# Performance work log

Hardware: AMD Instinct MI355X
Metric: run time of the kernel (lower is better)

## Reference

```python
import jax, jax.numpy as jnp
import numpy as np

EMBED_DIM = 768
VOCAB = 4096
HID = 128
B, N = 8, 4096


def setup_inputs() -> dict:
    key = jax.random.key(0)
    ks = jax.random.split(key, 12)
    s = lambda k, sh, fan_in: jax.random.normal(k, sh, jnp.float32) * (1.0 / np.sqrt(fan_in))
    return {
        "coordinates": jax.random.normal(ks[0], (B, N, 2), jnp.float32),
        "features": jax.random.normal(ks[1], (B, N, 10), jnp.float32),
        # spatial encoder: Linear(2,128) -> ReLU -> Linear(128,768); weights stored [in,out]
        "Ws1": s(ks[2], (2, HID), 2), "bs1": jnp.zeros((HID,), jnp.float32),
        "Ws2": s(ks[3], (HID, EMBED_DIM), HID), "bs2": jnp.zeros((EMBED_DIM,), jnp.float32),
        # feature encoder: Linear(10,128) -> ReLU -> Linear(128,768)
        "Wf1": s(ks[4], (10, HID), 10), "bf1": jnp.zeros((HID,), jnp.float32),
        "Wf2": s(ks[5], (HID, EMBED_DIM), HID), "bf2": jnp.zeros((EMBED_DIM,), jnp.float32),
        # quantizer codebook (nn.Embedding weight)
        "codebook": jax.random.normal(ks[6], (VOCAB, EMBED_DIM), jnp.float32),
    }


def reference(coordinates, features, Ws1, bs1, Ws2, bs2, Wf1, bf1, Wf2, bf2, codebook):
    spatial_emb = jax.nn.relu(coordinates @ Ws1 + bs1) @ Ws2 + bs2   # [B,N,D]
    feature_emb = jax.nn.relu(features @ Wf1 + bf1) @ Wf2 + bf2     # [B,N,D]
    combined = spatial_emb + feature_emb                             # [B,N,D]
    # squared euclidean distances (argmin is invariant to sqrt / -||x||^2 term)
    x_sq = jnp.sum(combined * combined, axis=-1, keepdims=True)      # [B,N,1]
    c_sq = jnp.sum(codebook * codebook, axis=-1)                     # [V]
    dots = jnp.einsum('bnd,vd->bnv', combined, codebook)             # [B,N,V]
    dists = x_sq - 2.0 * dots + c_sq                                 # [B,N,V]
    tokens = jnp.argmin(dists, axis=-1)                              # [B,N] int
    quantized = codebook[tokens]                                     # [B,N,D]
    return tokens, quantized
```

## Files before the change

kernel.cpp:

```cpp
#include <hip/hip_runtime.h>
#include <hip/hip_bf16.h>
#include <cfloat>

#define M_ROWS 32768
#define DIM    768
#define VOCABN 4096
#define HIDN   128
#define QB     64
#define CAP    32
#define MARGIN 2.0f

#define BM1 128
#define BN1 128
#define NCB (VOCABN / BN1)
#define CAP2 6
#define NKC  (DIM / 32)

typedef __attribute__((ext_vector_type(8))) short bf16x8;
typedef __attribute__((ext_vector_type(4))) float f32x4;

static __device__ __forceinline__ short f2b(float x) {
    __hip_bfloat16 h = __float2bfloat16(x);
    return *reinterpret_cast<short*>(&h);
}

static __device__ __forceinline__ void gload_lds16(const void* g, void* l) {
    __builtin_amdgcn_global_load_lds(
        (const __attribute__((address_space(1))) unsigned int*)g,
        (__attribute__((address_space(3))) unsigned int*)l, 16, 0, 0);
}


__global__ __launch_bounds__(256) void encode_kernel(
    const float* __restrict__ coords, const float* __restrict__ feats,
    const float* __restrict__ Ws1, const float* __restrict__ bs1,
    const float* __restrict__ Ws2, const float* __restrict__ bs2,
    const float* __restrict__ Wf1, const float* __restrict__ bf1,
    const float* __restrict__ Wf2, const float* __restrict__ bf2,
    float* __restrict__ comb, short* __restrict__ comb16f, int write16)
{
    __shared__ float hs[32][HIDN];
    __shared__ float hf[32][HIDN];
    const int row0 = blockIdx.x * 32;
    const int t = threadIdx.x;

    #pragma unroll
    for (int k = 0; k < 16; ++k) {
        const int idx = t + k * 256;
        const int r = idx >> 7;
        const int j = idx & 127;
        const int row = row0 + r;
        const float c0 = coords[row * 2 + 0];
        const float c1 = coords[row * 2 + 1];
        float vs = fmaf(c0, Ws1[j], fmaf(c1, Ws1[HIDN + j], bs1[j]));
        hs[r][j] = fmaxf(vs, 0.0f);
        float vf = bf1[j];
        #pragma unroll
        for (int i = 0; i < 10; ++i)
            vf = fmaf(feats[row * 10 + i], Wf1[i * HIDN + j], vf);
        hf[r][j] = fmaxf(vf, 0.0f);
    }
    __syncthreads();

    float acc[3][32];
    #pragma unroll
    for (int dd = 0; dd < 3; ++dd) {
        const float base = bs2[t + dd * 256] + bf2[t + dd * 256];
        #pragma unroll
        for (int r = 0; r < 32; ++r) acc[dd][r] = base;
    }

    for (int jq = 0; jq < 32; ++jq) {
        float ws[3][4], wf[3][4];
        #pragma unroll
        for (int dd = 0; dd < 3; ++dd) {
            const int d = t + dd * 256;
            #pragma unroll
            for (int jj = 0; jj < 4; ++jj) {
                ws[dd][jj] = Ws2[(jq * 4 + jj) * DIM + d];
                wf[dd][jj] = Wf2[(jq * 4 + jj) * DIM + d];
            }
        }
        #pragma unroll
        for (int r = 0; r < 32; ++r) {
            const float4 h4s = *(const float4*)&hs[r][jq * 4];
            const float4 h4f = *(const float4*)&hf[r][jq * 4];
            #pragma unroll
            for (int dd = 0; dd < 3; ++dd) {
                float a = acc[dd][r];
                a = fmaf(h4s.x, ws[dd][0], a);
                a = fmaf(h4s.y, ws[dd][1], a);
                a = fmaf(h4s.z, ws[dd][2], a);
                a = fmaf(h4s.w, ws[dd][3], a);
                a = fmaf(h4f.x, wf[dd][0], a);
                a = fmaf(h4f.y, wf[dd][1], a);
                a = fmaf(h4f.z, wf[dd][2], a);
                a = fmaf(h4f.w, wf[dd][3], a);
                acc[dd][r] = a;
            }
        }
    }

    const int qt = row0 >> 7;
    #pragma unroll
    for (int dd = 0; dd < 3; ++dd) {
        const int d = t + dd * 256;
        const int kc = d >> 5, kg = (d >> 3) & 3, jj = d & 7;
        #pragma unroll
        for (int r = 0; r < 32; ++r) {
            const int row = row0 + r;
            const float v = acc[dd][r];
            comb[(size_t)row * DIM + d] = v;
            if (write16) {
                const int it = (row >> 4) & 7, n = row & 15;
                const size_t unit = ((size_t)(qt * 8 + it) * NKC + kc) * 64 + kg * 16 + n;
                comb16f[unit * 8 + jj] = f2b(v);
            }
        }
    }
}

__global__ __launch_bounds__(64) void csq_cvt_kernel(
    const float* __restrict__ codebook, float* __restrict__ csq,
    short* __restrict__ outb, int swizzled)
{
    const int v = blockIdx.x;
    const int l = threadIdx.x;
    float s = 0.0f;
    #pragma unroll
    for (int k = 0; k < DIM / 64; ++k) {
        const float x = codebook[(size_t)v * DIM + l + k * 64];
        if (!swizzled) outb[(size_t)v * DIM + l + k * 64] = f2b(x);
        s = fmaf(x, x, s);
    }
    #pragma unroll
    for (int off = 32; off >= 1; off >>= 1)
        s += __shfl_down(s, off);
    if (l == 0) csq[v] = s;

    if (swizzled) {
        const int cb = v >> 7, jt = (v >> 4) & 7, n = v & 15;
        for (int u = l; u < 96; u += 64) {
            const int kc = u >> 2, kg = u & 3;
            const float* src = codebook + (size_t)v * DIM + kc * 32 + kg * 8;
            bf16x8 f;
            #pragma unroll
            for (int j = 0; j < 8; ++j) f[j] = f2b(src[j]);
            const size_t unit = ((size_t)(cb * 8 + jt) * NKC + kc) * 64 + kg * 16 + n;
            *(bf16x8*)(outb + unit * 8) = f;
        }
    }
}

__global__ __launch_bounds__(256, 3) void vq_phase1_kernel(
    const short* __restrict__ comb16f, const short* __restrict__ cbf,
    const float* __restrict__ csq,
    float* __restrict__ lmin_g, int* __restrict__ lbidx_g,
    int* __restrict__ lcnt_g, int* __restrict__ lci_g)
{
    __shared__ __align__(16) char smem[2 * 16384];

    const int t = threadIdx.x;
    const int w = t >> 6, l = t & 63;
    const int lm = l & 15, quad = l >> 4;
    const int wr = w >> 1, wc = w & 1;

    const int lin = blockIdx.y * (int)gridDim.x + blockIdx.x;
    const int x  = lin & 7;
    const int s_ = (lin >> 3) & 63;
    const int r_ = lin >> 9;
    const int qt = (r_ * 4 + (x >> 1)) * 4 + (s_ >> 4);
    const int cb = (x & 1) * 16 + (s_ & 15);
    const int q0 = qt * BM1;

    const short* gsrc[4];
    int doff[4];
    #pragma unroll
    for (int k = 0; k < 4; ++k) {
        const int s = w * 4 + k;
        if (s < 8) {
            gsrc[k] = comb16f + (((size_t)(qt * 8 + s) * NKC) * 64 + l) * 8;
            doff[k] = s * 1024;
        } else {
            gsrc[k] = cbf + (((size_t)(cb * 8 + (s - 8)) * NKC) * 64 + l) * 8;
            doff[k] = 8192 + (s - 8) * 1024;
        }
    }

    f32x4 acc[4][4];
    #pragma unroll
    for (int i = 0; i < 4; ++i)
        #pragma unroll
        for (int j = 0; j < 4; ++j) acc[i][j] = (f32x4){0.f, 0.f, 0.f, 0.f};

    #define STAGE(kc) do {                                                      \
        char* _d = smem + ((kc) & 1) * 16384;                                   \
        _Pragma("unroll")                                                       \
        for (int _k = 0; _k < 4; ++_k)                                          \
            gload_lds16(gsrc[_k] + (size_t)(kc) * 512, _d + doff[_k]);          \
    } while (0)

    STAGE(0);
    __syncthreads();

    #pragma unroll
    for (int kc = 0; kc < NKC; ++kc) {
        if (kc + 1 < NKC) STAGE(kc + 1);
        const char* buf = smem + (kc & 1) * 16384;
        bf16x8 a[4], b[4];
        #pragma unroll
        for (int i = 0; i < 4; ++i)
            a[i] = *(const bf16x8*)(buf + (wr * 4 + i) * 1024 + l * 16);
        #pragma unroll
        for (int j = 0; j < 4; ++j)
            b[j] = *(const bf16x8*)(buf + 8192 + (wc * 4 + j) * 1024 + l * 16);
        #pragma unroll
        for (int i = 0; i < 4; ++i)
            #pragma unroll
            for (int j = 0; j < 4; ++j)
                acc[i][j] = __builtin_amdgcn_mfma_f32_16x16x32_bf16(
                    a[i], b[j], acc[i][j], 0, 0, 0);
        if (kc + 1 < NKC) __syncthreads();
    }
    #undef STAGE

    float* s_wmin = (float*)smem;
    int*   s_widx = (int*)(smem + 1024);
    float* s_thr  = (float*)(smem + 2048);
    int*   s_cnt  = (int*)(smem + 2560);
    int*   s_ci   = (int*)(smem + 3072);

    __syncthreads();
    if (t < BM1) s_cnt[t] = 0;

    const int cbase = cb * BN1 + wc * 64;
    float cs[4];
    #pragma unroll
    for (int j = 0; j < 4; ++j) cs[j] = csq[cbase + j * 16 + lm];
    #pragma unroll
    for (int i = 0; i < 4; ++i)
        #pragma unroll
        for (int j = 0; j < 4; ++j)
            #pragma unroll
            for (int r = 0; r < 4; ++r)
                acc[i][j][r] = fmaf(-2.0f, acc[i][j][r], cs[j]);

    #pragma unroll
    for (int i = 0; i < 4; ++i)
        #pragma unroll
        for (int r = 0; r < 4; ++r) {
            float m = acc[i][0][r];
            int mi = cbase + 0 * 16 + lm;
            #pragma unroll
            for (int j = 1; j < 4; ++j) {
                const float d = acc[i][j][r];
                const int ci = cbase + j * 16 + lm;
                if (d < m || (d == m && ci < mi)) { m = d; mi = ci; }
            }
            #pragma unroll
            for (int off = 1; off <= 8; off <<= 1) {
                const float om = __shfl_xor(m, off);
                const int oi = __shfl_xor(mi, off);
                if (om < m || (om == m && oi < mi)) { m = om; mi = oi; }
            }
            if (lm == 0) {
                const int qloc = wr * 64 + i * 16 + quad * 4 + r;
                s_wmin[wc * 128 + qloc] = m;
                s_widx[wc * 128 + qloc] = mi;
            }
        }
    __syncthreads();

    if (t < BM1) {
        const float v0 = s_wmin[t], v1 = s_wmin[128 + t];
        const int i0 = s_widx[t], i1 = s_widx[128 + t];
        const float bm = fminf(v0, v1);
        const int bi = (v1 < v0 || (v1 == v0 && i1 < i0)) ? i1 : i0;
        const size_t base = (size_t)cb * M_ROWS + (q0 + t);
        lmin_g[base] = bm;
        lbidx_g[base] = bi;
        s_thr[t] = bm + MARGIN;
    }
    __syncthreads();

    #pragma unroll
    for (int i = 0; i < 4; ++i)
        #pragma unroll
        for (int r = 0; r < 4; ++r) {
            const int qloc = wr * 64 + i * 16 + quad * 4 + r;
            const float thr = s_thr[qloc];
            #pragma unroll
            for (int j = 0; j < 4; ++j) {
                const float d = acc[i][j][r];
                if (d <= thr) {
                    const int p = atomicAdd(&s_cnt[qloc], 1);
                    if (p < CAP2) s_ci[qloc * CAP2 + p] = cbase + j * 16 + lm;
                }
            }
        }
    __syncthreads();

    if (t < BM1) {
        const size_t base = (size_t)cb * M_ROWS + (q0 + t);
        const int raw = s_cnt[t];
        lcnt_g[base] = raw;
        int n = raw;
        if (n > CAP2) n = CAP2;
        for (int p = 0; p < n; ++p)
            lci_g[base * CAP2 + p] = s_ci[t * CAP2 + p];
    }
}

#define P2CAP 48
__global__ __launch_bounds__(256) void vq_phase2_kernel(
    const float* __restrict__ comb32, const float* __restrict__ codebook,
    const float* __restrict__ csq,
    const float* __restrict__ lmin_g, const int* __restrict__ lbidx_g,
    const int* __restrict__ lcnt_g, const int* __restrict__ lci_g,
    float* __restrict__ out_tok_f, float* __restrict__ out_q)
{
    __shared__ int s2n[4];
    __shared__ int s2c[4][P2CAP];
    const int t = threadIdx.x, w = t >> 6, l = t & 63;
    const int q = blockIdx.x * 4 + w;
    if (l == 0) s2n[w] = 0;

    const size_t base = (size_t)l * M_ROWS + q;
    const float v = (l < NCB) ? lmin_g[base] : FLT_MAX;
    float g = v;
    #pragma unroll
    for (int off = 1; off <= 32; off <<= 1)
        g = fminf(g, __shfl_xor(g, off));
    const float thr = g + MARGIN;

    if (l < NCB && v <= thr) {
        const int raw = lcnt_g[base];
        int n = raw;
        if (n > CAP2) n = CAP2;
        if (raw > CAP2) {
            const int p = atomicAdd(&s2n[w], 1);
            if (p < P2CAP) s2c[w][p] = lbidx_g[base];
        }
        for (int e = 0; e < n; ++e) {
            const int p = atomicAdd(&s2n[w], 1);
            if (p < P2CAP) s2c[w][p] = lci_g[base * CAP2 + e];
        }
    }
    __syncthreads();

    int ns = s2n[w];
    if (ns > P2CAP) ns = P2CAP;

    const float4* xr = (const float4*)(comb32 + (size_t)q * DIM);
    float4 xreg[3];
    #pragma unroll
    for (int k = 0; k < 3; ++k) xreg[k] = xr[l + 64 * k];

    float bestd = FLT_MAX;
    int bestc = 0x7fffffff;
    for (int e = 0; e < ns; e += 2) {
        const int c0 = s2c[w][e];
        const bool has1 = (e + 1 < ns);
        const int c1 = has1 ? s2c[w][e + 1] : c0;
        const float4* cr0 = (const float4*)(codebook + (size_t)c0 * DIM);
        const float4* cr1 = (const float4*)(codebook + (size_t)c1 * DIM);
        float dot0 = 0.0f, dot1 = 0.0f;
        #pragma unroll
        for (int k = 0; k < 3; ++k) {
            const float4 y0 = cr0[l + 64 * k];
            const float4 y1 = cr1[l + 64 * k];
            const float4 xk = xreg[k];
            dot0 = fmaf(xk.x, y0.x, fmaf(xk.y, y0.y, fmaf(xk.z, y0.z, fmaf(xk.w, y0.w, dot0))));
            dot1 = fmaf(xk.x, y1.x, fmaf(xk.y, y1.y, fmaf(xk.z, y1.z, fmaf(xk.w, y1.w, dot1))));
        }
        #pragma unroll
        for (int off = 1; off <= 32; off <<= 1) {
            dot0 += __shfl_xor(dot0, off);
            dot1 += __shfl_xor(dot1, off);
        }
        const float d0 = fmaf(-2.0f, dot0, csq[c0]);
        if (d0 < bestd || (d0 == bestd && c0 < bestc)) { bestd = d0; bestc = c0; }
        if (has1) {
            const float d1 = fmaf(-2.0f, dot1, csq[c1]);
            if (d1 < bestd || (d1 == bestd && c1 < bestc)) { bestd = d1; bestc = c1; }
        }
    }
    if (l == 0) out_tok_f[q] = (float)bestc;
    const float4* cr = (const float4*)(codebook + (size_t)bestc * DIM);
    float4* o4 = (float4*)(out_q + (size_t)q * DIM);
    #pragma unroll
    for (int k = 0; k < 3; ++k) o4[l + 64 * k] = cr[l + 64 * k];
}

__global__ __launch_bounds__(256) void argmin_mfma_kernel(
    const float* __restrict__ comb, const float* __restrict__ codebook,
    const short* __restrict__ cbb, const float* __restrict__ csq,
    float* __restrict__ out_tok_f, int* __restrict__ tok_i)
{
    __shared__ int s_cnt[QB];
    __shared__ int s_cand[QB][CAP];

    const int t = threadIdx.x;
    const int w = t >> 6;
    const int l = t & 63;
    const int lm = l & 15;
    const int quad = l >> 4;
    const int q0 = blockIdx.x * QB;

    for (int i = t; i < QB; i += 256) s_cnt[i] = 0;
    __syncthreads();

    bf16x8 a_reg[24];
    {
        const int qa = q0 + w * 16 + lm;
        const float* ap = comb + (size_t)qa * DIM + quad * 8;
        #pragma unroll
        for (int kc = 0; kc < 24; ++kc) {
            const float4 lo = *(const float4*)(ap + kc * 32);
            const float4 hi = *(const float4*)(ap + kc * 32 + 4);
            bf16x8 f;
            f[0] = f2b(lo.x); f[1] = f2b(lo.y); f[2] = f2b(lo.z); f[3] = f2b(lo.w);
            f[4] = f2b(hi.x); f[5] = f2b(hi.y); f[6] = f2b(hi.z); f[7] = f2b(hi.w);
            a_reg[kc] = f;
        }
    }

    const short* bp = cbb + (size_t)lm * DIM + quad * 8;
    float runmin[4] = {FLT_MAX, FLT_MAX, FLT_MAX, FLT_MAX};

    for (int chunk = 0; chunk < VOCABN / 64; ++chunk) {
        const int c0 = chunk * 64;
        const short* bc = bp + (size_t)c0 * DIM;
        f32x4 acc[4];
        #pragma unroll
        for (int s = 0; s < 4; ++s) acc[s] = (f32x4){0.f, 0.f, 0.f, 0.f};

        #pragma unroll
        for (int kc = 0; kc < 24; ++kc) {
            const bf16x8 a = a_reg[kc];
            #pragma unroll
            for (int s = 0; s < 4; ++s) {
                const bf16x8 b = *(const bf16x8*)(bc + s * 16 * DIM + kc * 32);
                acc[s] = __builtin_amdgcn_mfma_f32_16x16x32_bf16(a, b, acc[s], 0, 0, 0);
            }
        }

        float d[4][4];
        float m[4] = {FLT_MAX, FLT_MAX, FLT_MAX, FLT_MAX};
        #pragma unroll
        for (int s = 0; s < 4; ++s) {
            const float csv = csq[c0 + s * 16 + lm];
            #pragma unroll
            for (int r = 0; r < 4; ++r) {
                d[s][r] = fmaf(-2.0f, acc[s][r], csv);
                m[r] = fminf(m[r], d[s][r]);
            }
        }
        #pragma unroll
        for (int r = 0; r < 4; ++r) {
            float vv = m[r];
            vv = fminf(vv, __shfl_xor(vv, 1));
            vv = fminf(vv, __shfl_xor(vv, 2));
            vv = fminf(vv, __shfl_xor(vv, 4));
            vv = fminf(vv, __shfl_xor(vv, 8));
            runmin[r] = fminf(runmin[r], vv);
        }
        #pragma unroll
        for (int s = 0; s < 4; ++s) {
            #pragma unroll
            for (int r = 0; r < 4; ++r) {
                if (d[s][r] <= runmin[r] + MARGIN) {
                    const int qloc = w * 16 + quad * 4 + r;
                    const int idx = atomicAdd(&s_cnt[qloc], 1);
                    if (idx < CAP) s_cand[qloc][idx] = c0 + s * 16 + lm;
                }
            }
        }
    }
    __syncthreads();

    const int qloc = t >> 2;
    const int sub = t & 3;
    const int qg = q0 + qloc;
    int n = s_cnt[qloc];
    if (n > CAP) n = CAP;
    float bestd = FLT_MAX;
    int bestc = 0x7fffffff;
    const float4* xr = (const float4*)(comb + (size_t)qg * DIM);
    for (int i = 0; i < n; ++i) {
        const int c = s_cand[qloc][i];
        const float4* cr = (const float4*)(codebook + (size_t)c * DIM);
        float dot = 0.0f;
        #pragma unroll 4
        for (int j = sub * 48; j < sub * 48 + 48; ++j) {
            const float4 x = xr[j];
            const float4 y = cr[j];
            dot = fmaf(x.x, y.x, fmaf(x.y, y.y, fmaf(x.z, y.z, fmaf(x.w, y.w, dot))));
        }
        dot += __shfl_xor(dot, 1);
        dot += __shfl_xor(dot, 2);
        const float dist = fmaf(-2.0f, dot, csq[c]);
        if (dist < bestd || (dist == bestd && c < bestc)) { bestd = dist; bestc = c; }
    }
    if (sub == 0) {
        out_tok_f[qg] = (float)bestc;
        tok_i[qg] = bestc;
    }
}

__global__ __launch_bounds__(192) void gather_kernel(
    const int* __restrict__ tok, const float* __restrict__ codebook,
    float* __restrict__ outq)
{
    const int row = blockIdx.x;
    const int t = threadIdx.x;
    const int token = tok[row];
    const float4* cb4 = (const float4*)(codebook + (size_t)token * DIM);
    float4* o4 = (float4*)(outq + (size_t)row * DIM);
    o4[t] = cb4[t];
}

extern "C" void kernel_launch(void* const* d_in, const int* in_sizes, int n_in,
                              void* d_out, int out_size, void* d_ws, size_t ws_size,
                              hipStream_t stream) {
    const float* coords   = (const float*)d_in[0];
    const float* feats    = (const float*)d_in[1];
    const float* Ws1      = (const float*)d_in[2];
    const float* bs1      = (const float*)d_in[3];
    const float* Ws2      = (const float*)d_in[4];
    const float* bs2      = (const float*)d_in[5];
    const float* Wf1      = (const float*)d_in[6];
    const float* bf1      = (const float*)d_in[7];
    const float* Wf2      = (const float*)d_in[8];
    const float* bf2      = (const float*)d_in[9];
    const float* codebook = (const float*)d_in[10];

    float* out = (float*)d_out;
    float* out_tok = out;
    float* out_q   = out + M_ROWS;

    const size_t SZ_COMB32 = (size_t)M_ROWS * DIM * 4;
    const size_t SZ_COMB16 = (size_t)M_ROWS * DIM * 2;
    const size_t SZ_CBB    = (size_t)VOCABN * DIM * 2;
    const size_t SZ_CSQ    = (size_t)VOCABN * 4;
    const size_t SZ_LMIN   = (size_t)M_ROWS * NCB * 4;
    const size_t SZ_LCI    = (size_t)M_ROWS * NCB * CAP2 * 4;
    const size_t NEED = SZ_COMB32 + SZ_COMB16 + SZ_CBB + SZ_CSQ +
                        3 * SZ_LMIN + SZ_LCI;

    char* p = (char*)d_ws;
    float* comb32 = (float*)p;              p += SZ_COMB32;
    short* comb16f = (short*)p;             p += SZ_COMB16;
    short* cbx = (short*)p;                 p += SZ_CBB;
    float* csq = (float*)p;                 p += SZ_CSQ;

    if (ws_size >= NEED) {
        float* lmin_g = (float*)p;          p += SZ_LMIN;
        int*   lbidx_g = (int*)p;           p += SZ_LMIN;
        int*   lcnt_g = (int*)p;            p += SZ_LMIN;
        int*   lci_g = (int*)p;             p += SZ_LCI;

        encode_kernel<<<M_ROWS / 32, 256, 0, stream>>>(
            coords, feats, Ws1, bs1, Ws2, bs2, Wf1, bf1, Wf2, bf2,
            comb32, comb16f, 1);
        csq_cvt_kernel<<<VOCABN, 64, 0, stream>>>(codebook, csq, cbx, 1);
        dim3 g1(NCB, M_ROWS / BM1, 1);
        vq_phase1_kernel<<<g1, 256, 0, stream>>>(
            comb16f, cbx, csq, lmin_g, lbidx_g, lcnt_g, lci_g);
        vq_phase2_kernel<<<M_ROWS / 4, 256, 0, stream>>>(
            comb32, codebook, csq, lmin_g, lbidx_g, lcnt_g, lci_g,
            out_tok, out_q);
    } else {
        int* toki = (int*)p;
        encode_kernel<<<M_ROWS / 32, 256, 0, stream>>>(
            coords, feats, Ws1, bs1, Ws2, bs2, Wf1, bf1, Wf2, bf2,
            comb32, comb16f, 0);
        csq_cvt_kernel<<<VOCABN, 64, 0, stream>>>(codebook, csq, cbx, 0);
        argmin_mfma_kernel<<<M_ROWS / QB, 256, 0, stream>>>(
            comb32, codebook, cbx, csq, out_tok, toki);
        gather_kernel<<<M_ROWS, 192, 0, stream>>>(toki, codebook, out_q);
    }
}
```

Before: 616.5 us.

## Split encoder into hidden-layer and output-layer kernels for more parallelism

The fused encoder is replaced on the main path by two kernels. The first computes both ReLU hidden layers into a global buffer that aliases the phase-1 scratch. The second runs the 128→768 projection with 16 rows per block instead of 32, doubling the grid to 2048 blocks, and reads hidden values through scalar (readfirstlane) global loads instead of LDS. This aims for better occupancy and lower register pressure, at the cost of an extra launch and a global round-trip for the hidden activations. Reusing the lmin buffer is safe only because phase 1 overwrites it after the encoder finishes.

```diff
diff --git a/kernel.cpp b/kernel.cpp
--- a/kernel.cpp
+++ b/kernel.cpp
@@ -31,43 +31,45 @@
 }
 
 
-__global__ __launch_bounds__(256) void encode_kernel(
+__global__ __launch_bounds__(256) void encode_l1_kernel(
     const float* __restrict__ coords, const float* __restrict__ feats,
     const float* __restrict__ Ws1, const float* __restrict__ bs1,
-    const float* __restrict__ Ws2, const float* __restrict__ bs2,
     const float* __restrict__ Wf1, const float* __restrict__ bf1,
-    const float* __restrict__ Wf2, const float* __restrict__ bf2,
-    float* __restrict__ comb, short* __restrict__ comb16f, int write16)
-{
-    __shared__ float hs[32][HIDN];
-    __shared__ float hf[32][HIDN];
-    const int row0 = blockIdx.x * 32;
-    const int t = threadIdx.x;
-
-    #pragma unroll
-    for (int k = 0; k < 16; ++k) {
-        const int idx = t + k * 256;
-        const int r = idx >> 7;
+    float* __restrict__ hbuf)
+{
+    const int tid0 = blockIdx.x * 256 + threadIdx.x;
+    #pragma unroll
+    for (int it = 0; it < 8; ++it) {
+        const int idx = tid0 + it * 524288;
+        const int row = idx >> 7;
         const int j = idx & 127;
-        const int row = row0 + r;
         const float c0 = coords[row * 2 + 0];
         const float c1 = coords[row * 2 + 1];
-        float vs = fmaf(c0, Ws1[j], fmaf(c1, Ws1[HIDN + j], bs1[j]));
-        hs[r][j] = fmaxf(vs, 0.0f);
+        const float vs = fmaf(c0, Ws1[j], fmaf(c1, Ws1[HIDN + j], bs1[j]));
         float vf = bf1[j];
         #pragma unroll
         for (int i = 0; i < 10; ++i)
             vf = fmaf(feats[row * 10 + i], Wf1[i * HIDN + j], vf);
-        hf[r][j] = fmaxf(vf, 0.0f);
-    }
-    __syncthreads();
-
-    float acc[3][32];
+        hbuf[(size_t)row * 256 + j] = fmaxf(vs, 0.0f);
+        hbuf[(size_t)row * 256 + 128 + j] = fmaxf(vf, 0.0f);
+    }
+}
+
+__global__ __launch_bounds__(256) void encode_l2_kernel(
+    const float* __restrict__ hbuf,
+    const float* __restrict__ Ws2, const float* __restrict__ bs2,
+    const float* __restrict__ Wf2, const float* __restrict__ bf2,
+    float* __restrict__ comb, short* __restrict__ comb16f)
+{
+    const int rows0 = blockIdx.x * 16;
+    const int t = threadIdx.x;
+
+    float acc[3][16];
     #pragma unroll
     for (int dd = 0; dd < 3; ++dd) {
         const float base = bs2[t + dd * 256] + bf2[t + dd * 256];
         #pragma unroll
-        for (int r = 0; r < 32; ++r) acc[dd][r] = base;
+        for (int r = 0; r < 16; ++r) acc[dd][r] = base;
     }
 
     for (int jq = 0; jq < 32; ++jq) {
@@ -82,9 +84,11 @@
             }
         }
         #pragma unroll
-        for (int r = 0; r < 32; ++r) {
-            const float4 h4s = *(const float4*)&hs[r][jq * 4];
-            const float4 h4f = *(const float4*)&hf[r][jq * 4];
+        for (int r = 0; r < 16; ++r) {
+            const int off = __builtin_amdgcn_readfirstlane(
+                (rows0 + r) * 256 + jq * 4);
+            const float4 h4s = *(const float4*)(hbuf + off);
+            const float4 h4f = *(const float4*)(hbuf + off + 128);
             #pragma unroll
             for (int dd = 0; dd < 3; ++dd) {
                 float a = acc[dd][r];
@@ -101,7 +105,92 @@
         }
     }
 
-    const int qt = row0 >> 7;
+    #pragma unroll
+    for (int dd = 0; dd < 3; ++dd) {
+        const int d = t + dd * 256;
+        const int kc = d >> 5, kg = (d >> 3) & 3, jj = d & 7;
+        #pragma unroll
+        for (int r = 0; r < 16; ++r) {
+            const int row = rows0 + r;
+            const float v = acc[dd][r];
+            comb[(size_t)row * DIM + d] = v;
+            const size_t unit =
+                ((size_t)(row >> 4) * NKC + kc) * 64 + kg * 16 + (row & 15);
+            comb16f[unit * 8 + jj] = f2b(v);
+        }
+    }
+}
+
+__global__ __launch_bounds__(256) void encode_kernel(
+    const float* __restrict__ coords, const float* __restrict__ feats,
+    const float* __restrict__ Ws1, const float* __restrict__ bs1,
+    const float* __restrict__ Ws2, const float* __restrict__ bs2,
+    const float* __restrict__ Wf1, const float* __restrict__ bf1,
+    const float* __restrict__ Wf2, const float* __restrict__ bf2,
+    float* __restrict__ comb, short* __restrict__ comb16f, int write16)
+{
+    __shared__ float hs[32][HIDN];
+    __shared__ float hf[32][HIDN];
+    const int row0 = blockIdx.x * 32;
+    const int t = threadIdx.x;
+
+    #pragma unroll
+    for (int k = 0; k < 16; ++k) {
+        const int idx = t + k * 256;
+        const int r = idx >> 7;
+        const int j = idx & 127;
+        const int row = row0 + r;
+        const float c0 = coords[row * 2 + 0];
+        const float c1 = coords[row * 2 + 1];
+        float vs = fmaf(c0, Ws1[j], fmaf(c1, Ws1[HIDN + j], bs1[j]));
+        hs[r][j] = fmaxf(vs, 0.0f);
+        float vf = bf1[j];
+        #pragma unroll
+        for (int i = 0; i < 10; ++i)
+            vf = fmaf(feats[row * 10 + i], Wf1[i * HIDN + j], vf);
+        hf[r][j] = fmaxf(vf, 0.0f);
+    }
+    __syncthreads();
+
+    float acc[3][32];
+    #pragma unroll
+    for (int dd = 0; dd < 3; ++dd) {
+        const float base = bs2[t + dd * 256] + bf2[t + dd * 256];
+        #pragma unroll
+        for (int r = 0; r < 32; ++r) acc[dd][r] = base;
+    }
+
+    for (int jq = 0; jq < 32; ++jq) {
+        float ws[3][4], wf[3][4];
+        #pragma unroll
+        for (int dd = 0; dd < 3; ++dd) {
+            const int d = t + dd * 256;
+            #pragma unroll
+            for (int jj = 0; jj < 4; ++jj) {
+                ws[dd][jj] = Ws2[(jq * 4 + jj) * DIM + d];
+                wf[dd][jj] = Wf2[(jq * 4 + jj) * DIM + d];
+            }
+        }
+        #pragma unroll
+        for (int r = 0; r < 32; ++r) {
+            const float4 h4s = *(const float4*)&hs[r][jq * 4];
+            const float4 h4f = *(const float4*)&hf[r][jq * 4];
+            #pragma unroll
+            for (int dd = 0; dd < 3; ++dd) {
+                float a = acc[dd][r];
+                a = fmaf(h4s.x, ws[dd][0], a);
+                a = fmaf(h4s.y, ws[dd][1], a);
+                a = fmaf(h4s.z, ws[dd][2], a);
+                a = fmaf(h4s.w, ws[dd][3], a);
+                a = fmaf(h4f.x, wf[dd][0], a);
+                a = fmaf(h4f.y, wf[dd][1], a);
+                a = fmaf(h4f.z, wf[dd][2], a);
+                a = fmaf(h4f.w, wf[dd][3], a);
+                acc[dd][r] = a;
+            }
+        }
+    }
+
     #pragma unroll
     for (int dd = 0; dd < 3; ++dd) {
         const int d = t + dd * 256;
@@ -112,8 +201,8 @@
             const float v = acc[dd][r];
             comb[(size_t)row * DIM + d] = v;
             if (write16) {
-                const int it = (row >> 4) & 7, n = row & 15;
-                const size_t unit = ((size_t)(qt * 8 + it) * NKC + kc) * 64 + kg * 16 + n;
+                const size_t unit =
+                    ((size_t)(row >> 4) * NKC + kc) * 64 + kg * 16 + (row & 15);
                 comb16f[unit * 8 + jj] = f2b(v);
             }
         }
@@ -560,9 +649,12 @@
         int*   lcnt_g = (int*)p;            p += SZ_LMIN;
         int*   lci_g = (int*)p;             p += SZ_LCI;
 
-        encode_kernel<<<M_ROWS / 32, 256, 0, stream>>>(
-            coords, feats, Ws1, bs1, Ws2, bs2, Wf1, bf1, Wf2, bf2,
-            comb32, comb16f, 1);
+        float* hbuf = lmin_g;
+
+        encode_l1_kernel<<<2048, 256, 0, stream>>>(
+            coords, feats, Ws1, bs1, Wf1, bf1, hbuf);
+        encode_l2_kernel<<<2048, 256, 0, stream>>>(
+            hbuf, Ws2, bs2, Wf2, bf2, comb32, comb16f);
         csq_cvt_kernel<<<VOCABN, 64, 0, stream>>>(codebook, csq, cbx, 1);
         dim3 g1(NCB, M_ROWS / BM1, 1);
         vq_phase1_kernel<<<g1, 256, 0, stream>>>(
```

Measured after the change: 693.0 us. 12.4% more time.
